# Performance work log

Measured on AMD Instinct MI355X. Metric: run time of the kernel, lower is better.

## Reference

```python
import jax, jax.numpy as jnp
import numpy as np

N_NODES, N_EDGES, D_IN, D_OUT = 50000, 400000, 512, 512


def setup_inputs() -> dict:
    key = jax.random.key(0)
    k = jax.random.split(key, 7)
    s = 1.0 / np.sqrt(D_IN)
    return {
        "x": jax.random.normal(k[0], (N_NODES, D_IN), dtype=jnp.float32),
        "src": jax.random.randint(k[1], (N_EDGES,), 0, N_NODES),
        "dst": jax.random.randint(k[2], (N_EDGES,), 0, N_NODES),
        "W1": jax.random.uniform(k[3], (D_IN, D_OUT), jnp.float32, -s, s),
        "b1": jax.random.uniform(k[4], (D_OUT,), jnp.float32, -s, s),
        "W2": jax.random.uniform(k[5], (D_IN, D_OUT), jnp.float32, -s, s),
        "b2": jax.random.uniform(k[6], (D_OUT,), jnp.float32, -s, s),
    }


def reference(x, src, dst, W1, b1, W2, b2):
    n_nodes = x.shape[0]
    # gather src features along each edge, segment-sum into dst nodes
    msg_sum = jax.ops.segment_sum(x[src], dst, num_segments=n_nodes)      # [N, D_in]
    counts = jax.ops.segment_sum(jnp.ones_like(dst, dtype=x.dtype), dst,
                                 num_segments=n_nodes)                    # [N]
    mean = msg_sum / jnp.maximum(counts, 1.0)[:, None]                    # mailbox mean
    out = (x @ W1 + b1) + ((x - mean) @ W2 + b2)
    # DGL update_all leaves nodes with no incoming messages untouched
    return jnp.where((counts > 0)[:, None], out, x)
```

## Files before the change

kernel.cpp:

```cpp
#include <hip/hip_runtime.h>
#include <hip/hip_bf16.h>
#include <stdint.h>

typedef unsigned short u16;
typedef unsigned int   u32;

#define N_NODES 50000
#define N_EDGES 400000
#define DDIM    512

typedef __attribute__((ext_vector_type(8))) __bf16 bf16x8;
typedef __attribute__((ext_vector_type(4))) float  f32x4;

__device__ __forceinline__ float bflo(u32 d) { return __builtin_bit_cast(float, d << 16); }
__device__ __forceinline__ float bfhi(u32 d) { return __builtin_bit_cast(float, d & 0xffff0000u); }
__device__ __forceinline__ u16 f2bf(float f) {
    u32 u = __builtin_bit_cast(u32, f);
    u32 r = u + 0x7fffu + ((u >> 16) & 1u);
    return (u16)(r >> 16);
}
__device__ __forceinline__ u32 pack2(float a, float b) {
    return (u32)f2bf(a) | ((u32)f2bf(b) << 16);
}
__device__ __forceinline__ void gload_lds16(const void* g, void* l) {
    __builtin_amdgcn_global_load_lds(
        (const __attribute__((address_space(1))) void*)g,
        (__attribute__((address_space(3))) void*)l, 16, 0, 0);
}

__global__ void cvt_k(const float* __restrict__ x, u16* __restrict__ xb) {
    int i = blockIdx.x * 256 + threadIdx.x;
    const float4* p = (const float4*)(x + (size_t)i * 8);
    float4 a = p[0], b = p[1];
    uint4 o;
    o.x = pack2(a.x, a.y); o.y = pack2(a.z, a.w);
    o.z = pack2(b.x, b.y); o.w = pack2(b.z, b.w);
    ((uint4*)xb)[i] = o;
}

__global__ void hist_k(const int* __restrict__ dst, int* __restrict__ counts) {
    int e = blockIdx.x * 256 + threadIdx.x;
    if (e < N_EDGES) atomicAdd(&counts[dst[e]], 1);
}

#define NCHUNK 49
__global__ __launch_bounds__(1024) void scanA_k(const int* __restrict__ counts, int* __restrict__ csum) {
    __shared__ int ws[16];
    int t = threadIdx.x, b = blockIdx.x;
    int i = b * 1024 + t;
    int v = (i < N_NODES) ? counts[i] : 0;
    for (int d = 32; d; d >>= 1) v += __shfl_down(v, d);
    if ((t & 63) == 0) ws[t >> 6] = v;
    __syncthreads();
    if (t < 16) {
        int s = ws[t];
        for (int d = 8; d; d >>= 1) s += __shfl_down(s, d);
        if (t == 0) csum[b] = s;
    }
}
__global__ void scanB_k(int* __restrict__ csum) {
    int t = threadIdx.x;
    int v = (t < NCHUNK) ? csum[t] : 0;
    int s = v;
    for (int d = 1; d < 64; d <<= 1) { int u = __shfl_up(s, d); if (t >= d) s += u; }
    if (t < NCHUNK) csum[t] = s - v;
}
__global__ __launch_bounds__(1024) void scanC_k(const int* __restrict__ counts, const int* __restrict__ csum,
                                                int* __restrict__ offsets, int* __restrict__ cursor) {
    __shared__ int wsum[16];
    int t = threadIdx.x, b = blockIdx.x;
    int i = b * 1024 + t;
    int lane = t & 63, w = t >> 6;
    int v = (i < N_NODES) ? counts[i] : 0;
    int s = v;
    for (int d = 1; d < 64; d <<= 1) { int u = __shfl_up(s, d); if (lane >= d) s += u; }
    if (lane == 63) wsum[w] = s;
    __syncthreads();
    if (t < 16) {
        int ww = wsum[t], ss = ww;
        for (int d = 1; d < 16; d <<= 1) { int u = __shfl_up(ss, d); if (t >= d) ss += u; }
        wsum[t] = ss - ww;
    }
    __syncthreads();
    int excl = (s - v) + wsum[w] + csum[b];
    if (i < N_NODES) { offsets[i] = excl; cursor[i] = excl; }
}

__global__ void fill_k(const int* __restrict__ src, const int* __restrict__ dst,
                       int* __restrict__ cursor, int* __restrict__ esrc) {
    int e = blockIdx.x * 256 + threadIdx.x;
    if (e < N_EDGES) {
        int d = dst[e];
        int p = atomicAdd(&cursor[d], 1);
        esrc[p] = src[e];
    }
}

__global__ void prepw_k(const float* __restrict__ W1, const float* __restrict__ W2,
                        const float* __restrict__ b1, const float* __restrict__ b2,
                        u16* __restrict__ Wt12, u16* __restrict__ Wt2, float* __restrict__ b12) {
    int idx = blockIdx.x * 256 + threadIdx.x;
    int k = idx >> 9, n = idx & 511;
    float w1 = W1[idx], w2 = W2[idx];
    Wt12[n * 512 + k] = f2bf(w1 + w2);
    Wt2[n * 512 + k]  = f2bf(w2);
    if (idx < 512) b12[idx] = b1[idx] + b2[idx];
}

__device__ __forceinline__ void addrow(float* acc, uint4 v) {
    acc[0] += bflo(v.x); acc[1] += bfhi(v.x);
    acc[2] += bflo(v.y); acc[3] += bfhi(v.y);
    acc[4] += bflo(v.z); acc[5] += bfhi(v.z);
    acc[6] += bflo(v.w); acc[7] += bfhi(v.w);
}
__global__ __launch_bounds__(256) void agg_k(const u16* __restrict__ xb,
                                             const int* __restrict__ offsets,
                                             const int* __restrict__ counts,
                                             const int* __restrict__ esrc,
                                             u16* __restrict__ meanNeg) {
    int nid = blockIdx.x * 4 + (threadIdx.x >> 6);
    if (nid >= N_NODES) return;
    int lane = threadIdx.x & 63;
    int off = offsets[nid], deg = counts[nid];
    float acc[8] = {0, 0, 0, 0, 0, 0, 0, 0};
    int e = 0;
    for (; e + 3 < deg; e += 4) {
        int s0 = esrc[off + e], s1 = esrc[off + e + 1];
        int s2 = esrc[off + e + 2], s3 = esrc[off + e + 3];
        uint4 v0 = *(const uint4*)(xb + (size_t)s0 * DDIM + lane * 8);
        uint4 v1 = *(const uint4*)(xb + (size_t)s1 * DDIM + lane * 8);
        uint4 v2 = *(const uint4*)(xb + (size_t)s2 * DDIM + lane * 8);
        uint4 v3 = *(const uint4*)(xb + (size_t)s3 * DDIM + lane * 8);
        addrow(acc, v0); addrow(acc, v1); addrow(acc, v2); addrow(acc, v3);
    }
    for (; e < deg; e++) {
        int s0 = esrc[off + e];
        addrow(acc, *(const uint4*)(xb + (size_t)s0 * DDIM + lane * 8));
    }
    float scale = (deg > 0) ? (-1.0f / (float)deg) : 0.0f;
    uint4 o;
    o.x = pack2(acc[0] * scale, acc[1] * scale);
    o.y = pack2(acc[2] * scale, acc[3] * scale);
    o.z = pack2(acc[4] * scale, acc[5] * scale);
    o.w = pack2(acc[6] * scale, acc[7] * scale);
    *(uint4*)(meanNeg + (size_t)nid * DDIM + lane * 8) = o;
}

__global__ __launch_bounds__(256) void gemm_k(const u16* __restrict__ xb,
                                              const float* __restrict__ x,
                                              const u16* __restrict__ meanNeg,
                                              const u16* __restrict__ Wt12,
                                              const u16* __restrict__ Wt2,
                                              const float* __restrict__ b12,
                                              const int* __restrict__ counts,
                                              float* __restrict__ out) {
    __shared__ u16 As[128 * 32];
    __shared__ u16 Bs[128 * 32];
    const int m0 = blockIdx.x * 128;
    const int n0 = blockIdx.y * 128;
    const int tid = threadIdx.x;
    const int lane = tid & 63;
    const int wid  = tid >> 6;
    const int wm = wid >> 1, wn = wid & 1;
    const int quad = lane >> 4, lr = lane & 15;

    f32x4 acc[4][4] = {};

    const int skoff = (lane & 3) * 8;
    const int srsub = lane >> 2;
    int arow[2], brow[2];
    #pragma unroll
    for (int t = 0; t < 2; t++) {
        int r = wid * 32 + t * 16 + srsub;
        int ar = m0 + r; if (ar >= N_NODES) ar = N_NODES - 1;
        arow[t] = ar;
        brow[t] = n0 + r;
    }

    for (int pass = 0; pass < 2; pass++) {
        const u16* __restrict__ A = pass ? meanNeg : xb;
        const u16* __restrict__ B = pass ? Wt2 : Wt12;
        for (int k0 = 0; k0 < 512; k0 += 32) {
            #pragma unroll
            for (int t = 0; t < 2; t++) {
                int rblk = wid * 32 + t * 16;
                gload_lds16(A + (size_t)arow[t] * DDIM + k0 + skoff, &As[rblk * 32]);
                gload_lds16(B + (size_t)brow[t] * DDIM + k0 + skoff, &Bs[rblk * 32]);
            }
            __syncthreads();
            bf16x8 af[4], bfr[4];
            #pragma unroll
            for (int i = 0; i < 4; i++)
                af[i] = *(const bf16x8*)&As[(wm * 64 + i * 16 + lr) * 32 + quad * 8];
            #pragma unroll
            for (int j = 0; j < 4; j++)
                bfr[j] = *(const bf16x8*)&Bs[(wn * 64 + j * 16 + lr) * 32 + quad * 8];
            #pragma unroll
            for (int i = 0; i < 4; i++)
                #pragma unroll
                for (int j = 0; j < 4; j++)
                    acc[i][j] = __builtin_amdgcn_mfma_f32_16x16x32_bf16(af[i], bfr[j], acc[i][j], 0, 0, 0);
            __syncthreads();
        }
    }

    #pragma unroll
    for (int i = 0; i < 4; i++) {
        #pragma unroll
        for (int r = 0; r < 4; r++) {
            int grow = m0 + wm * 64 + i * 16 + quad * 4 + r;
            if (grow >= N_NODES) continue;
            int cnt = counts[grow];
            #pragma unroll
            for (int j = 0; j < 4; j++) {
                int gcol = n0 + wn * 64 + j * 16 + lr;
                float v;
                if (cnt > 0) v = acc[i][j][r] + b12[gcol];
                else         v = x[(size_t)grow * DDIM + gcol];
                out[(size_t)grow * DDIM + gcol] = v;
            }
        }
    }
}

extern "C" void kernel_launch(void* const* d_in, const int* in_sizes, int n_in,
                              void* d_out, int out_size, void* d_ws, size_t ws_size,
                              hipStream_t stream) {
    const float* x  = (const float*)d_in[0];
    const int* src  = (const int*)d_in[1];
    const int* dst  = (const int*)d_in[2];
    const float* W1 = (const float*)d_in[3];
    const float* b1 = (const float*)d_in[4];
    const float* W2 = (const float*)d_in[5];
    const float* b2 = (const float*)d_in[6];
    float* out = (float*)d_out;

    char* ws = (char*)d_ws;
    size_t o = 0;
    auto alloc = [&](size_t bytes) { char* p = ws + o; o += (bytes + 255) & ~(size_t)255; return p; };
    int* counts   = (int*)alloc((size_t)N_NODES * 4);
    int* offsets  = (int*)alloc((size_t)N_NODES * 4);
    int* cursor   = (int*)alloc((size_t)N_NODES * 4);
    int* csum     = (int*)alloc((size_t)NCHUNK * 4);
    int* esrc     = (int*)alloc((size_t)N_EDGES * 4);
    u16* Wt12     = (u16*)alloc((size_t)512 * 512 * 2);
    u16* Wt2      = (u16*)alloc((size_t)512 * 512 * 2);
    float* b12    = (float*)alloc((size_t)512 * 4);
    u16* xb       = (u16*)alloc((size_t)N_NODES * DDIM * 2);
    u16* meanNeg  = (u16*)alloc((size_t)N_NODES * DDIM * 2);
    (void)ws_size; (void)n_in; (void)in_sizes; (void)out_size;

    hipMemsetAsync(counts, 0, (size_t)N_NODES * 4, stream);
    cvt_k<<<(N_NODES * DDIM / 8) / 256, 256, 0, stream>>>(x, xb);
    hist_k<<<(N_EDGES + 255) / 256, 256, 0, stream>>>(dst, counts);
    scanA_k<<<NCHUNK, 1024, 0, stream>>>(counts, csum);
    scanB_k<<<1, 64, 0, stream>>>(csum);
    scanC_k<<<NCHUNK, 1024, 0, stream>>>(counts, csum, offsets, cursor);
    fill_k<<<(N_EDGES + 255) / 256, 256, 0, stream>>>(src, dst, cursor, esrc);
    prepw_k<<<(512 * 512) / 256, 256, 0, stream>>>(W1, W2, b1, b2, Wt12, Wt2, b12);
    agg_k<<<(N_NODES + 3) / 4, 256, 0, stream>>>(xb, offsets, counts, esrc, meanNeg);
    gemm_k<<<dim3((N_NODES + 127) / 128, DDIM / 128), 256, 0, stream>>>(
        xb, x, meanNeg, Wt12, Wt2, b12, counts, out);
}
```

Measured before the change: 437.2 us.

## Concatenate GEMM operands, double-buffer LDS with swizzle, remap blocks per XCD

The x and negated-mean activations are stored interleaved in one [N,1024] bf16 buffer and the two weight matrices in one [512,1024] buffer, so the GEMM becomes a single K=1024 loop. The GEMM moves to BK=64 with double-buffered LDS tiles, an XOR swizzle to cut bank conflicts, and a 1D grid remapped so adjacent tiles land on the same XCD for L2 reuse. The aim is to overlap global-to-LDS loads with MFMA work and halve barrier count per K step. The cost is doubled LDS use (64KB per block) and a strided activation layout, which gives the gather in the aggregation kernel a 2KB row stride.

Result: faster. 417.2 us (-4.6%).

```diff
diff --git a/kernel.cpp b/kernel.cpp
--- a/kernel.cpp
+++ b/kernel.cpp
@@ -8,6 +8,12 @@
 #define N_NODES 50000
 #define N_EDGES 400000
 #define DDIM    512
+#define KTOT    1024
+#define BM      128
+#define BN      128
+#define BK      64
+#define NT      (KTOT / BK)
+#define GRID_M  ((N_NODES + BM - 1) / BM)
 
 typedef __attribute__((ext_vector_type(8))) __bf16 bf16x8;
 typedef __attribute__((ext_vector_type(4))) float  f32x4;
@@ -28,14 +34,15 @@
         (__attribute__((address_space(3))) void*)l, 16, 0, 0);
 }
 
-__global__ void cvt_k(const float* __restrict__ x, u16* __restrict__ xb) {
+__global__ void cvt_k(const float* __restrict__ x, u16* __restrict__ Acat) {
     int i = blockIdx.x * 256 + threadIdx.x;
-    const float4* p = (const float4*)(x + (size_t)i * 8);
+    int node = i >> 6, c8 = i & 63;
+    const float4* p = (const float4*)(x + (size_t)node * DDIM + c8 * 8);
     float4 a = p[0], b = p[1];
     uint4 o;
     o.x = pack2(a.x, a.y); o.y = pack2(a.z, a.w);
     o.z = pack2(b.x, b.y); o.w = pack2(b.z, b.w);
-    ((uint4*)xb)[i] = o;
+    *(uint4*)(Acat + (size_t)node * KTOT + c8 * 8) = o;
 }
 
 __global__ void hist_k(const int* __restrict__ dst, int* __restrict__ counts) {
@@ -98,12 +105,12 @@
 
 __global__ void prepw_k(const float* __restrict__ W1, const float* __restrict__ W2,
                         const float* __restrict__ b1, const float* __restrict__ b2,
-                        u16* __restrict__ Wt12, u16* __restrict__ Wt2, float* __restrict__ b12) {
+                        u16* __restrict__ Wcat, float* __restrict__ b12) {
     int idx = blockIdx.x * 256 + threadIdx.x;
     int k = idx >> 9, n = idx & 511;
     float w1 = W1[idx], w2 = W2[idx];
-    Wt12[n * 512 + k] = f2bf(w1 + w2);
-    Wt2[n * 512 + k]  = f2bf(w2);
+    Wcat[(size_t)n * KTOT + k]       = f2bf(w1 + w2);
+    Wcat[(size_t)n * KTOT + 512 + k] = f2bf(w2);
     if (idx < 512) b12[idx] = b1[idx] + b2[idx];
 }
 
@@ -113,11 +120,10 @@
     acc[4] += bflo(v.z); acc[5] += bfhi(v.z);
     acc[6] += bflo(v.w); acc[7] += bfhi(v.w);
 }
-__global__ __launch_bounds__(256) void agg_k(const u16* __restrict__ xb,
+__global__ __launch_bounds__(256) void agg_k(u16* Acat,
                                              const int* __restrict__ offsets,
                                              const int* __restrict__ counts,
-                                             const int* __restrict__ esrc,
-                                             u16* __restrict__ meanNeg) {
+                                             const int* __restrict__ esrc) {
     int nid = blockIdx.x * 4 + (threadIdx.x >> 6);
     if (nid >= N_NODES) return;
     int lane = threadIdx.x & 63;
@@ -127,15 +133,15 @@
     for (; e + 3 < deg; e += 4) {
         int s0 = esrc[off + e], s1 = esrc[off + e + 1];
         int s2 = esrc[off + e + 2], s3 = esrc[off + e + 3];
-        uint4 v0 = *(const uint4*)(xb + (size_t)s0 * DDIM + lane * 8);
-        uint4 v1 = *(const uint4*)(xb + (size_t)s1 * DDIM + lane * 8);
-        uint4 v2 = *(const uint4*)(xb + (size_t)s2 * DDIM + lane * 8);
-        uint4 v3 = *(const uint4*)(xb + (size_t)s3 * DDIM + lane * 8);
+        uint4 v0 = *(const uint4*)(Acat + (size_t)s0 * KTOT + lane * 8);
+        uint4 v1 = *(const uint4*)(Acat + (size_t)s1 * KTOT + lane * 8);
+        uint4 v2 = *(const uint4*)(Acat + (size_t)s2 * KTOT + lane * 8);
+        uint4 v3 = *(const uint4*)(Acat + (size_t)s3 * KTOT + lane * 8);
         addrow(acc, v0); addrow(acc, v1); addrow(acc, v2); addrow(acc, v3);
     }
     for (; e < deg; e++) {
         int s0 = esrc[off + e];
-        addrow(acc, *(const uint4*)(xb + (size_t)s0 * DDIM + lane * 8));
+        addrow(acc, *(const uint4*)(Acat + (size_t)s0 * KTOT + lane * 8));
     }
     float scale = (deg > 0) ? (-1.0f / (float)deg) : 0.0f;
     uint4 o;
@@ -143,65 +149,91 @@
     o.y = pack2(acc[2] * scale, acc[3] * scale);
     o.z = pack2(acc[4] * scale, acc[5] * scale);
     o.w = pack2(acc[6] * scale, acc[7] * scale);
-    *(uint4*)(meanNeg + (size_t)nid * DDIM + lane * 8) = o;
-}
-
-__global__ __launch_bounds__(256) void gemm_k(const u16* __restrict__ xb,
-                                              const float* __restrict__ x,
-                                              const u16* __restrict__ meanNeg,
-                                              const u16* __restrict__ Wt12,
-                                              const u16* __restrict__ Wt2,
-                                              const float* __restrict__ b12,
-                                              const int* __restrict__ counts,
-                                              float* __restrict__ out) {
-    __shared__ u16 As[128 * 32];
-    __shared__ u16 Bs[128 * 32];
-    const int m0 = blockIdx.x * 128;
-    const int n0 = blockIdx.y * 128;
-    const int tid = threadIdx.x;
+    *(uint4*)(Acat + (size_t)nid * KTOT + 512 + lane * 8) = o;
+}
+
+__global__ __launch_bounds__(256, 2) void gemm_k(const u16* __restrict__ Acat,
+                                                 const float* __restrict__ x,
+                                                 const u16* __restrict__ Wcat,
+                                                 const float* __restrict__ b12,
+                                                 const int* __restrict__ counts,
+                                                 float* __restrict__ out) {
+    __shared__ u16 As[2][BM * BK];
+    __shared__ u16 Bs[2][BN * BK];
+
+    const int nwg = gridDim.x;
+    int orig = blockIdx.x;
+    int xcd = orig & 7, loc = orig >> 3;
+    int q8 = nwg >> 3, r8 = nwg & 7;
+    int wg = (xcd < r8 ? xcd * (q8 + 1) : r8 * (q8 + 1) + (xcd - r8) * q8) + loc;
+    const int m0 = (wg >> 2) * BM;
+    const int n0 = (wg & 3) * BN;
+
+    const int tid  = threadIdx.x;
     const int lane = tid & 63;
     const int wid  = tid >> 6;
     const int wm = wid >> 1, wn = wid & 1;
     const int quad = lane >> 4, lr = lane & 15;
 
+    const int srow = tid >> 3;
+    const int so8  = (((tid & 7) ^ (srow & 7)) << 3);
+    int arowg[4], browg[4];
+    #pragma unroll
+    for (int q = 0; q < 4; q++) {
+        int r = q * 32 + srow;
+        int ar = m0 + r; if (ar > N_NODES - 1) ar = N_NODES - 1;
+        arowg[q] = ar;
+        browg[q] = n0 + r;
+    }
+
     f32x4 acc[4][4] = {};
 
-    const int skoff = (lane & 3) * 8;
-    const int srsub = lane >> 2;
-    int arow[2], brow[2];
-    #pragma unroll
-    for (int t = 0; t < 2; t++) {
-        int r = wid * 32 + t * 16 + srsub;
-        int ar = m0 + r; if (ar >= N_NODES) ar = N_NODES - 1;
-        arow[t] = ar;
-        brow[t] = n0 + r;
-    }
-
-    for (int pass = 0; pass < 2; pass++) {
-        const u16* __restrict__ A = pass ? meanNeg : xb;
-        const u16* __restrict__ B = pass ? Wt2 : Wt12;
-        for (int k0 = 0; k0 < 512; k0 += 32) {
-            #pragma unroll
-            for (int t = 0; t < 2; t++) {
-                int rblk = wid * 32 + t * 16;
-                gload_lds16(A + (size_t)arow[t] * DDIM + k0 + skoff, &As[rblk * 32]);
-                gload_lds16(B + (size_t)brow[t] * DDIM + k0 + skoff, &Bs[rblk * 32]);
-            }
-            __syncthreads();
-            bf16x8 af[4], bfr[4];
+    auto stage = [&](u16* Asb, u16* Bsb, int t) {
+        const int k0 = t * BK;
+        #pragma unroll
+        for (int q = 0; q < 4; q++) {
+            gload_lds16(Acat + (size_t)arowg[q] * KTOT + k0 + so8,
+                        Asb + q * 2048 + wid * 512);
+            gload_lds16(Wcat + (size_t)browg[q] * KTOT + k0 + so8,
+                        Bsb + q * 2048 + wid * 512);
+        }
+    };
+
+    const int swb   = (lr & 7) << 4;
+    const int arow0 = (wm * 64 + lr) * 128;
+    const int brow0 = (wn * 64 + lr) * 128;
+
+    auto compute = [&](const u16* Asb, const u16* Bsb) {
+        bf16x8 af[2][4], bfr[2][4];
+        #pragma unroll
+        for (int ks = 0; ks < 2; ks++) {
+            const int koff = (ks * 64 + quad * 16) ^ swb;
             #pragma unroll
             for (int i = 0; i < 4; i++)
-                af[i] = *(const bf16x8*)&As[(wm * 64 + i * 16 + lr) * 32 + quad * 8];
+                af[ks][i] = *(const bf16x8*)((const char*)Asb + arow0 + i * 2048 + koff);
             #pragma unroll
             for (int j = 0; j < 4; j++)
-                bfr[j] = *(const bf16x8*)&Bs[(wn * 64 + j * 16 + lr) * 32 + quad * 8];
+                bfr[ks][j] = *(const bf16x8*)((const char*)Bsb + brow0 + j * 2048 + koff);
+        }
+        #pragma unroll
+        for (int ks = 0; ks < 2; ks++)
             #pragma unroll
             for (int i = 0; i < 4; i++)
                 #pragma unroll
                 for (int j = 0; j < 4; j++)
-                    acc[i][j] = __builtin_amdgcn_mfma_f32_16x16x32_bf16(af[i], bfr[j], acc[i][j], 0, 0, 0);
-            __syncthreads();
-        }
+                    acc[i][j] = __builtin_amdgcn_mfma_f32_16x16x32_bf16(af[ks][i], bfr[ks][j], acc[i][j], 0, 0, 0);
+    };
+
+    stage(As[0], Bs[0], 0);
+    __syncthreads();
+    #pragma unroll 1
+    for (int t = 0; t < NT; t += 2) {
+        stage(As[1], Bs[1], t + 1);
+        compute(As[0], Bs[0]);
+        __syncthreads();
+        if (t + 2 < NT) stage(As[0], Bs[0], t + 2);
+        compute(As[1], Bs[1]);
+        __syncthreads();
     }
 
     #pragma unroll
@@ -243,22 +275,19 @@
     int* cursor   = (int*)alloc((size_t)N_NODES * 4);
     int* csum     = (int*)alloc((size_t)NCHUNK * 4);
     int* esrc     = (int*)alloc((size_t)N_EDGES * 4);
-    u16* Wt12     = (u16*)alloc((size_t)512 * 512 * 2);
-    u16* Wt2      = (u16*)alloc((size_t)512 * 512 * 2);
+    u16* Wcat     = (u16*)alloc((size_t)512 * KTOT * 2);
     float* b12    = (float*)alloc((size_t)512 * 4);
-    u16* xb       = (u16*)alloc((size_t)N_NODES * DDIM * 2);
-    u16* meanNeg  = (u16*)alloc((size_t)N_NODES * DDIM * 2);
+    u16* Acat     = (u16*)alloc((size_t)N_NODES * KTOT * 2);
     (void)ws_size; (void)n_in; (void)in_sizes; (void)out_size;
 
     hipMemsetAsync(counts, 0, (size_t)N_NODES * 4, stream);
-    cvt_k<<<(N_NODES * DDIM / 8) / 256, 256, 0, stream>>>(x, xb);
+    cvt_k<<<(N_NODES * 64) / 256, 256, 0, stream>>>(x, Acat);
     hist_k<<<(N_EDGES + 255) / 256, 256, 0, stream>>>(dst, counts);
     scanA_k<<<NCHUNK, 1024, 0, stream>>>(counts, csum);
     scanB_k<<<1, 64, 0, stream>>>(csum);
     scanC_k<<<NCHUNK, 1024, 0, stream>>>(counts, csum, offsets, cursor);
     fill_k<<<(N_EDGES + 255) / 256, 256, 0, stream>>>(src, dst, cursor, esrc);
-    prepw_k<<<(512 * 512) / 256, 256, 0, stream>>>(W1, W2, b1, b2, Wt12, Wt2, b12);
-    agg_k<<<(N_NODES + 3) / 4, 256, 0, stream>>>(xb, offsets, counts, esrc, meanNeg);
-    gemm_k<<<dim3((N_NODES + 127) / 128, DDIM / 128), 256, 0, stream>>>(
-        xb, x, meanNeg, Wt12, Wt2, b12, counts, out);
-}
+    prepw_k<<<(512 * 512) / 256, 256, 0, stream>>>(W1, W2, b1, b2, Wcat, b12);
+    agg_k<<<(N_NODES + 3) / 4, 256, 0, stream>>>(Acat, offsets, counts, esrc);
+    gemm_k<<<dim3(GRID_M * 4), 256, 0, stream>>>(Acat, x, Wcat, b12, counts, out);
+}
```
